# Kernel tuning notes

Measured on AMD Instinct MI355X. Metric: run time of the kernel, lower is better.

Reference implementation:

```python
import jax, jax.numpy as jnp
import numpy as np

B, S, H, NH = 2, 2048, 1024, 16
DK = H // NH

def setup_inputs() -> dict:
    key = jax.random.key(0)
    ks = jax.random.split(key, 12)
    scale = 0.02
    return {
        "Q": jax.random.normal(ks[0], (B, S, H), jnp.float32),
        "K": jax.random.normal(ks[1], (B, S, H), jnp.float32),
        "V": jax.random.normal(ks[2], (B, S, H), jnp.float32),
        "attn_mask": jax.random.randint(ks[3], (B, S, S), 0, 2).astype(bool),
        "Wq": jax.random.normal(ks[4], (H, H), jnp.float32) * scale,
        "bq": jnp.zeros((H,), jnp.float32),
        "Wk": jax.random.normal(ks[5], (H, H), jnp.float32) * scale,
        "bk": jnp.zeros((H,), jnp.float32),
        "Wv": jax.random.normal(ks[6], (H, H), jnp.float32) * scale,
        "bv": jnp.zeros((H,), jnp.float32),
        "Wo": jax.random.normal(ks[7], (H, H), jnp.float32) * scale,
        "bo": jnp.zeros((H,), jnp.float32),
    }

def reference(Q, K, V, attn_mask, Wq, bq, Wk, bk, Wv, bv, Wo, bo):
    b = Q.shape[0]
    # linear projections (torch nn.Linear: x @ W.T + b), split heads -> [b, nh, s, dk]
    def proj(x, W, bias):
        return (x @ W.T + bias).reshape(b, -1, NH, DK).transpose(0, 2, 1, 3)
    q = proj(Q, Wq, bq)
    k = proj(K, Wk, bk)
    v = proj(V, Wv, bv)
    scores = jnp.einsum("bhqd,bhkd->bhqk", q, k) / jnp.sqrt(jnp.float32(DK))
    scores = jnp.where(attn_mask[:, None, :, :], jnp.float32(-1e9), scores)
    attn = jax.nn.softmax(scores, axis=-1)  # dropout prob = 0.0 (identity)
    ctx = jnp.einsum("bhqk,bhkd->bhqd", attn, v)
    ctx = ctx.transpose(0, 2, 1, 3).reshape(b, -1, NH * DK)
    return ctx @ Wo.T + bo
```

## Files before the change

### kernel.cpp

```cpp
#include <hip/hip_runtime.h>

typedef short s16x8 __attribute__((ext_vector_type(8)));
typedef float f32x4 __attribute__((ext_vector_type(4)));
typedef unsigned short u16;
typedef unsigned int u32;
typedef unsigned long long u64;

#define DEVI __device__ __forceinline__

#if __has_builtin(__builtin_amdgcn_exp2f)
#define EXP2F(x) __builtin_amdgcn_exp2f(x)
#else
#define EXP2F(x) exp2f(x)
#endif

#define QSCALE 0.1803368801111204f

DEVI float bf2f(u16 u){ union { u32 i; float f; } v; v.i = ((u32)u) << 16; return v.f; }
DEVI u16 f2bf(float f){ union { float f; u32 i; } v; v.f = f; u32 u = v.i;
                        return (u16)((u + 0x7fffu + ((u >> 16) & 1u)) >> 16); }
DEVI u32 pack2r(float a, float b){
  union { float f; u32 i; } ua, ub; ua.f = a; ub.f = b;
  return ((ua.i + 0x8000u) >> 16) | ((ub.i + 0x8000u) & 0xffff0000u);
}
DEVI u64 pack4(float a, float b, float c, float d){
  return (u64)f2bf(a) | ((u64)f2bf(b) << 16) | ((u64)f2bf(c) << 32) | ((u64)f2bf(d) << 48);
}

DEVI f32x4 mfma_bf16(s16x8 a, s16x8 b, f32x4 c){
  return __builtin_amdgcn_mfma_f32_16x16x32_bf16(a, b, c, 0, 0, 0);
}

#define GLDS(gp, lp) __builtin_amdgcn_global_load_lds( \
    (const __attribute__((address_space(1))) void*)(gp), \
    (__attribute__((address_space(3))) void*)(lp), 16, 0, 0)

DEVI float4 cvt8f32(const float* p){
  float4 x = *(const float4*)p;
  float4 y = *(const float4*)(p + 4);
  union { u16 t[8]; float4 f4; } u;
  u.t[0] = f2bf(x.x); u.t[1] = f2bf(x.y); u.t[2] = f2bf(x.z); u.t[3] = f2bf(x.w);
  u.t[4] = f2bf(y.x); u.t[5] = f2bf(y.y); u.t[6] = f2bf(y.z); u.t[7] = f2bf(y.w);
  return u.f4;
}

DEVI bool detect_f32(const u16* probe){
  __shared__ int dsum[4];
  const int tid = threadIdx.x;
  int bad = 0;
#pragma unroll
  for (int i = 0; i < 16; ++i){
    u16 u = probe[tid * 16 + i];
    int e = (u >> 7) & 0xFF;
    bad += (e != 0 && (e < 100 || e > 150)) ? 1 : 0;
  }
#pragma unroll
  for (int o = 1; o < 64; o <<= 1) bad += __shfl_xor(bad, o);
  if ((tid & 63) == 0) dsum[tid >> 6] = bad;
  __syncthreads();
  bool r = (dsum[0] + dsum[1] + dsum[2] + dsum[3]) > 64;
  __syncthreads();
  return r;
}

struct PrepArgs { const void* src[7]; void* dst[7]; u32 coff[8]; };

__global__ __launch_bounds__(256) void prep_mask(PrepArgs a, const u16* probe,
                                                 const int* __restrict__ mask,
                                                 u64* __restrict__ bits,
                                                 int do_mask, int do_conv){
  if (blockIdx.x < 1024){
    if (!do_mask) return;
    const int lane = threadIdx.x & 63, wid = threadIdx.x >> 6;
    const int row = blockIdx.x * 4 + wid;
    const int* mrow = mask + (size_t)row * 2048;
    for (int c = 0; c < 32; ++c){
      int v = mrow[c * 64 + lane];
      u64 w = __ballot(v == 0);
      if (lane == 0) bits[(size_t)row * 32 + c] = w;
    }
  } else {
    if (!do_conv) return;
    const bool f32 = detect_f32(probe);
    if (!f32) return;
    const u32 total = a.coff[7];
    for (u32 c = (blockIdx.x - 1024) * 256 + threadIdx.x; c < total; c += 2048 * 256){
      int s = 0;
#pragma unroll
      for (int i = 1; i < 7; ++i) s += (c >= a.coff[i]) ? 1 : 0;
      u32 lc = c - a.coff[s];
      ((float4*)a.dst[s])[lc] = cvt8f32((const float*)a.src[s] + (size_t)lc * 8);
    }
  }
}

struct ProjP {
  const void* X[3];   const u16* Xc[3];
  const void* W[3];   const u16* Wc[3];
  const void* bias[3];
  u16* out[3];
  const u16* probe;
  int conv_ok;
};

__global__ __launch_bounds__(256) void proj_gemm(ProjP p){
  __shared__ u16 As[128 * 64];
  __shared__ u16 Bs[128 * 64];
  const int z = blockIdx.z;
  const bool in32 = detect_f32(p.probe);
  const bool f32st = in32 && !p.conv_ok;
  const u16* Ab = (in32 && p.conv_ok) ? p.Xc[z] : (const u16*)p.X[z];
  const u16* Wb = (in32 && p.conv_ok) ? p.Wc[z] : (const u16*)p.W[z];
  const float* Af = (const float*)p.X[z];
  const float* Wf = (const float*)p.W[z];
  const int tid = threadIdx.x;
  const int lane = tid & 63, wid = tid >> 6;
  const int quad = lane >> 4, l15 = lane & 15;
  const int m0 = blockIdx.y * 128, n0 = blockIdx.x * 128;
  const int wm = (wid >> 1) * 64, wn = (wid & 1) * 64;
  const int K = 1024;

  f32x4 acc[4][4];
  const f32x4 z4 = {0.f, 0.f, 0.f, 0.f};
  for (int i = 0; i < 4; ++i) for (int j = 0; j < 4; ++j) acc[i][j] = z4;

  for (int ko = 0; ko < 16; ++ko){
    const int kk = ko * 64;
    if (f32st){
#pragma unroll
      for (int i = 0; i < 4; ++i){
        int g = tid * 4 + i;
        int row = g >> 3, c = g & 7;
        *(float4*)(As + row * 64 + ((c ^ (row & 7)) * 8)) =
            cvt8f32(Af + (size_t)(m0 + row) * K + kk + c * 8);
        *(float4*)(Bs + row * 64 + ((c ^ (row & 7)) * 8)) =
            cvt8f32(Wf + (size_t)(n0 + row) * K + kk + c * 8);
      }
    } else {
#pragma unroll
      for (int i = 0; i < 4; ++i){
        int ci = (wid * 4 + i) * 64 + lane;
        int row = ci >> 3, gcc = (ci & 7) ^ (row & 7);
        GLDS(Ab + (size_t)(m0 + row) * K + kk + gcc * 8, As + (size_t)(wid * 4 + i) * 512);
        GLDS(Wb + (size_t)(n0 + row) * K + kk + gcc * 8, Bs + (size_t)(wid * 4 + i) * 512);
      }
    }
    __syncthreads();
#pragma unroll
    for (int ks = 0; ks < 2; ++ks){
      s16x8 af[4], bfr[4];
#pragma unroll
      for (int mt = 0; mt < 4; ++mt){
        int row = wm + mt * 16 + l15;
        af[mt] = *(const s16x8*)(As + row * 64 + (((ks * 4 + quad) ^ (row & 7)) * 8));
      }
#pragma unroll
      for (int nt = 0; nt < 4; ++nt){
        int row = wn + nt * 16 + l15;
        bfr[nt] = *(const s16x8*)(Bs + row * 64 + (((ks * 4 + quad) ^ (row & 7)) * 8));
      }
#pragma unroll
      for (int mt = 0; mt < 4; ++mt)
#pragma unroll
        for (int nt = 0; nt < 4; ++nt)
          acc[mt][nt] = mfma_bf16(af[mt], bfr[nt], acc[mt][nt]);
    }
    __syncthreads();
  }

  u16* outp = p.out[z];
#pragma unroll
  for (int nt = 0; nt < 4; ++nt){
    int col = n0 + wn + nt * 16 + l15;
    float bv = in32 ? ((const float*)p.bias[z])[col] : bf2f(((const u16*)p.bias[z])[col]);
#pragma unroll
    for (int mt = 0; mt < 4; ++mt){
      if (z == 2){
        int srow = m0 + wm + mt * 16 + quad * 4;
        int b = srow >> 11, s = srow & 2047, hh = col >> 6, d = col & 63;
        size_t idx = (((size_t)(b * 16 + hh)) * 64 + d) * 2048 + s;
        *(u64*)(outp + idx) = pack4(acc[mt][nt][0] + bv, acc[mt][nt][1] + bv,
                                    acc[mt][nt][2] + bv, acc[mt][nt][3] + bv);
      } else {
#pragma unroll
        for (int r = 0; r < 4; ++r){
          int row = m0 + wm + mt * 16 + quad * 4 + r;
          float v = acc[mt][nt][r] + bv;
          if (z == 0) v *= QSCALE;
          int b = row >> 11, s = row & 2047, hh = col >> 6, d = col & 63;
          outp[(((size_t)(b * 16 + hh)) * 2048 + s) * 64 + d] = f2bf(v);
        }
      }
    }
  }
}

__global__ __launch_bounds__(256) void gemm_out(const u16* __restrict__ A,
                                                const void* __restrict__ Wv,
                                                const u16* __restrict__ Wbf,
                                                const void* __restrict__ biasv,
                                                void* __restrict__ outv,
                                                const u16* __restrict__ probe,
                                                int conv_ok){
  __shared__ u16 As[64 * 64];
  __shared__ u16 Bs[64 * 64];
  const bool in32 = detect_f32(probe);
  const bool f32st = in32 && !conv_ok;
  const u16* Wb = (in32 && conv_ok) ? Wbf : (const u16*)Wv;
  const float* Wf = (const float*)Wv;
  const int tid = threadIdx.x;
  const int lane = tid & 63, wid = tid >> 6;
  const int quad = lane >> 4, l15 = lane & 15;
  const int m0 = blockIdx.y * 64, n0 = blockIdx.x * 64;
  const int wm = (wid >> 1) * 32, wn = (wid & 1) * 32;
  const int K = 1024;

  f32x4 acc[2][2];
  const f32x4 z4 = {0.f, 0.f, 0.f, 0.f};
  for (int i = 0; i < 2; ++i) for (int j = 0; j < 2; ++j) acc[i][j] = z4;

  for (int ko = 0; ko < 16; ++ko){
    const int kk = ko * 64;
#pragma unroll
    for (int i = 0; i < 2; ++i){
      int ci = (wid * 2 + i) * 64 + lane;
      int row = ci >> 3, gcc = (ci & 7) ^ (row & 7);
      GLDS(A + (size_t)(m0 + row) * K + kk + gcc * 8, As + (size_t)(wid * 2 + i) * 512);
    }
    if (f32st){
#pragma unroll
      for (int i = 0; i < 2; ++i){
        int g = tid * 2 + i;
        int row = g >> 3, c = g & 7;
        *(float4*)(Bs + row * 64 + ((c ^ (row & 7)) * 8)) =
            cvt8f32(Wf + (size_t)(n0 + row) * K + kk + c * 8);
      }
    } else {
#pragma unroll
      for (int i = 0; i < 2; ++i){
        int ci = (wid * 2 + i) * 64 + lane;
        int row = ci >> 3, gcc = (ci & 7) ^ (row & 7);
        GLDS(Wb + (size_t)(n0 + row) * K + kk + gcc * 8, Bs + (size_t)(wid * 2 + i) * 512);
      }
    }
    __syncthreads();
#pragma unroll
    for (int ks = 0; ks < 2; ++ks){
      s16x8 af[2], bfr[2];
#pragma unroll
      for (int mt = 0; mt < 2; ++mt){
        int row = wm + mt * 16 + l15;
        af[mt] = *(const s16x8*)(As + row * 64 + (((ks * 4 + quad) ^ (row & 7)) * 8));
      }
#pragma unroll
      for (int nt = 0; nt < 2; ++nt){
        int row = wn + nt * 16 + l15;
        bfr[nt] = *(const s16x8*)(Bs + row * 64 + (((ks * 4 + quad) ^ (row & 7)) * 8));
      }
#pragma unroll
      for (int mt = 0; mt < 2; ++mt)
#pragma unroll
        for (int nt = 0; nt < 2; ++nt)
          acc[mt][nt] = mfma_bf16(af[mt], bfr[nt], acc[mt][nt]);
    }
    __syncthreads();
  }

#pragma unroll
  for (int nt = 0; nt < 2; ++nt){
    int col = n0 + wn + nt * 16 + l15;
    float bv = in32 ? ((const float*)biasv)[col] : bf2f(((const u16*)biasv)[col]);
#pragma unroll
    for (int mt = 0; mt < 2; ++mt)
#pragma unroll
      for (int r = 0; r < 4; ++r){
        int row = m0 + wm + mt * 16 + quad * 4 + r;
        float v = acc[mt][nt][r] + bv;
        size_t idx = (size_t)row * 1024 + col;
        if (in32) ((float*)outv)[idx] = v;
        else      ((u16*)outv)[idx]   = f2bf(v);
      }
  }
}

__global__ __launch_bounds__(256) void attn2(const u16* __restrict__ qws,
                                             const u16* __restrict__ kws,
                                             const u16* __restrict__ vtws,
                                             const u64* __restrict__ mbits,
                                             const int* __restrict__ rawmask,
                                             int use_raw,
                                             u16* __restrict__ ctxws){
  __shared__ u16 Ks[64 * 64];
  __shared__ u16 Vt[64 * 64];
  __shared__ u16 Ps[4][16 * 64];
  const int tid = threadIdx.x;
  const int lane = tid & 63, wid = tid >> 6;
  const int quad = lane >> 4, l15 = lane & 15;
  const int h = blockIdx.x, qt = blockIdx.y, b = blockIdx.z;
  const int q0 = qt * 64;
  const size_t bh = (size_t)(b * 16 + h) * (2048 * 64);
  const int qrow = q0 + wid * 16 + l15;

  s16x8 qf[2];
#pragma unroll
  for (int ks = 0; ks < 2; ++ks)
    qf[ks] = *(const s16x8*)(qws + bh + (size_t)qrow * 64 + ks * 32 + quad * 8);

  const f32x4 z4 = {0.f, 0.f, 0.f, 0.f};
  f32x4 ctx[4];
  for (int dt = 0; dt < 4; ++dt) ctx[dt] = z4;
  float lr = 0.f;

  u16* pp = &Ps[wid][0];
  u32 pw[4];
#pragma unroll
  for (int ntk = 0; ntk < 4; ++ntk)
    pw[ntk] = l15 * 64 + (((u32)(ntk * 2 + (quad >> 1)) ^ (u32)(l15 & 7)) * 8) + (quad & 1) * 4;

  const u64* mrow = mbits + ((size_t)(b * 2048 + qrow)) * 32;

  for (int kt = 0; kt < 32; ++kt){
    const int k0 = kt * 64;
#pragma unroll
    for (int i = 0; i < 2; ++i){
      int ci = (wid * 2 + i) * 64 + lane;
      int row = ci >> 3, gcc = (ci & 7) ^ (row & 7);
      GLDS(kws + bh + (size_t)(k0 + row) * 64 + gcc * 8, Ks + (size_t)(wid * 2 + i) * 512);
      GLDS(vtws + bh + (size_t)row * 2048 + k0 + gcc * 8, Vt + (size_t)(wid * 2 + i) * 512);
    }
    __syncthreads();

    f32x4 s[4];
    for (int ntk = 0; ntk < 4; ++ntk) s[ntk] = z4;
#pragma unroll
    for (int ks = 0; ks < 2; ++ks)
#pragma unroll
      for (int ntk = 0; ntk < 4; ++ntk){
        int row = ntk * 16 + l15;
        s16x8 kf = *(const s16x8*)(Ks + row * 64 + (((ks * 4 + quad) ^ (row & 7)) * 8));
        s[ntk] = mfma_bf16(kf, qf[ks], s[ntk]);
      }

    float ls = 0.f;
    if (!use_raw){
      u64 w = mrow[kt] >> (quad * 4);
      u32 wlo = (u32)w, whi = (u32)(w >> 32);
#pragma unroll
      for (int ntk = 0; ntk < 4; ++ntk){
        u32 half = (ntk < 2) ? wlo : whi;
#pragma unroll
        for (int r = 0; r < 4; ++r){
          float pv = EXP2F(s[ntk][r]);
          u32 bit = (half >> ((ntk & 1) * 16 + r)) & 1u;
          pv *= (float)bit;
          s[ntk][r] = pv;
          ls += pv;
        }
      }
    } else {
#pragma unroll
      for (int ntk = 0; ntk < 4; ++ntk)
#pragma unroll
        for (int r = 0; r < 4; ++r){
          int key = k0 + ntk * 16 + quad * 4 + r;
          int mv = rawmask[((size_t)(b * 2048 + qrow)) * 2048 + key];
          float pv = EXP2F(s[ntk][r]);
          pv = mv ? 0.f : pv;
          s[ntk][r] = pv;
          ls += pv;
        }
    }
    lr += ls;

#pragma unroll
    for (int ntk = 0; ntk < 4; ++ntk){
      uint2 t;
      t.x = pack2r(s[ntk][0], s[ntk][1]);
      t.y = pack2r(s[ntk][2], s[ntk][3]);
      *(uint2*)(pp + pw[ntk]) = t;
    }
    s16x8 pf[2];
#pragma unroll
    for (int ks = 0; ks < 2; ++ks)
      pf[ks] = *(const s16x8*)(pp + l15 * 64 + (((ks * 4 + quad) ^ (l15 & 7)) * 8));

#pragma unroll
    for (int ks = 0; ks < 2; ++ks)
#pragma unroll
      for (int dt = 0; dt < 4; ++dt){
        int row = dt * 16 + l15;
        s16x8 vf = *(const s16x8*)(Vt + row * 64 + (((ks * 4 + quad) ^ (row & 7)) * 8));
        ctx[dt] = mfma_bf16(vf, pf[ks], ctx[dt]);
      }
    __syncthreads();
  }

  lr += __shfl_xor(lr, 16);
  lr += __shfl_xor(lr, 32);
  float inv = 1.0f / fmaxf(lr, 1e-30f);

#pragma unroll
  for (int dt = 0; dt < 4; ++dt){
    int d0 = dt * 16 + quad * 4;
    u64 w = pack4(ctx[dt][0] * inv, ctx[dt][1] * inv, ctx[dt][2] * inv, ctx[dt][3] * inv);
    *(u64*)(ctxws + ((size_t)(b * 2048 + qrow)) * 1024 + h * 64 + d0) = w;
  }
}

extern "C" void kernel_launch(void* const* d_in, const int* in_sizes, int n_in,
                              void* d_out, int out_size, void* d_ws, size_t ws_size,
                              hipStream_t stream){
  const void* Q    = d_in[0];
  const void* Kin  = d_in[1];
  const void* Vin  = d_in[2];
  const int* mask  = (const int*)d_in[3];
  const void* Wq = d_in[4];  const void* bq = d_in[5];
  const void* Wk = d_in[6];  const void* bk = d_in[7];
  const void* Wv = d_in[8];  const void* bv = d_in[9];
  const void* Wo = d_in[10]; const void* bo = d_in[11];

  char* ws = (char*)d_ws;
  const size_t MB = 1u << 20;
  const bool small_ws = ws_size < 33 * MB;
  const bool big_ws   = ws_size >= 66 * MB;
  u64* mbits = (u64*)ws;
  const size_t base = small_ws ? 0 : MB;
  u16* qws  = (u16*)(ws + base);
  u16* kws  = (u16*)(ws + base + 8 * MB);
  u16* vtws = (u16*)(ws + base + 16 * MB);
  u16* cws  = (u16*)(ws + base + 24 * MB);
  u16* Qc  = (u16*)(ws + 33 * MB);
  u16* Kc  = (u16*)(ws + 41 * MB);
  u16* Vc  = (u16*)(ws + 49 * MB);
  u16* Wqc = (u16*)(ws + 57 * MB);
  u16* Wkc = (u16*)(ws + 59 * MB);
  u16* Wvc = (u16*)(ws + 61 * MB);
  u16* Woc = (u16*)(ws + 63 * MB);
  const u16* probe = (const u16*)Q;

  PrepArgs pa;
  pa.src[0] = Q;  pa.src[1] = Kin; pa.src[2] = Vin;
  pa.src[3] = Wq; pa.src[4] = Wk;  pa.src[5] = Wv; pa.src[6] = Wo;
  pa.dst[0] = Qc;  pa.dst[1] = Kc;  pa.dst[2] = Vc;
  pa.dst[3] = Wqc; pa.dst[4] = Wkc; pa.dst[5] = Wvc; pa.dst[6] = Woc;
  const u32 cq = 4194304 / 8, cw = 1048576 / 8;
  pa.coff[0] = 0;
  pa.coff[1] = cq;          pa.coff[2] = 2 * cq;      pa.coff[3] = 3 * cq;
  pa.coff[4] = 3 * cq + cw; pa.coff[5] = 3 * cq + 2 * cw;
  pa.coff[6] = 3 * cq + 3 * cw; pa.coff[7] = 3 * cq + 4 * cw;
  prep_mask<<<dim3(3072), 256, 0, stream>>>(pa, probe, mask, mbits,
                                            small_ws ? 0 : 1, big_ws ? 1 : 0);

  ProjP pp;
  pp.X[0] = Q;  pp.X[1] = Kin; pp.X[2] = Vin;
  pp.Xc[0] = Qc; pp.Xc[1] = Kc; pp.Xc[2] = Vc;
  pp.W[0] = Wq; pp.W[1] = Wk; pp.W[2] = Wv;
  pp.Wc[0] = Wqc; pp.Wc[1] = Wkc; pp.Wc[2] = Wvc;
  pp.bias[0] = bq; pp.bias[1] = bk; pp.bias[2] = bv;
  pp.out[0] = qws; pp.out[1] = kws; pp.out[2] = vtws;
  pp.probe = probe;
  pp.conv_ok = big_ws ? 1 : 0;
  proj_gemm<<<dim3(8, 32, 3), 256, 0, stream>>>(pp);

  attn2<<<dim3(16, 32, 2), 256, 0, stream>>>(qws, kws, vtws, mbits, mask,
                                             small_ws ? 1 : 0, cws);

  gemm_out<<<dim3(16, 64), 256, 0, stream>>>(cws, Wo, Woc, bo, d_out, probe,
                                             big_ws ? 1 : 0);
}
```

Baseline: 282.7 us.

## Double-buffer K/V shared tiles in attention to prefetch the next tile

Splits the K and V^T shared-memory tiles into two buffers. The global-to-LDS loads for tile kt+1 are issued right after the barrier at the top of iteration kt, so they overlap with the QK^T, softmax and PV MFMA work on tile kt. The barrier at the end of the loop is removed, leaving one barrier per iteration. This doubles LDS use for K/V, which may reduce occupancy. The compiler may also insert conservative waits on the pending LDS loads that cancel the overlap.

```diff
diff --git a/kernel.cpp b/kernel.cpp
--- a/kernel.cpp
+++ b/kernel.cpp
@@ -290,8 +290,8 @@
                                              const int* __restrict__ rawmask,
                                              int use_raw,
                                              u16* __restrict__ ctxws){
-  __shared__ u16 Ks[64 * 64];
-  __shared__ u16 Vt[64 * 64];
+  __shared__ u16 Ks[2][64 * 64];
+  __shared__ u16 Vt[2][64 * 64];
   __shared__ u16 Ps[4][16 * 64];
   const int tid = threadIdx.x;
   const int lane = tid & 63, wid = tid >> 6;
@@ -319,16 +319,40 @@
 
   const u64* mrow = mbits + ((size_t)(b * 2048 + qrow)) * 32;
 
+  const int sci = wid * 2;
+  int srow0, sgc0, srow1, sgc1;
+  {
+    int ci0 = sci * 64 + lane;
+    srow0 = ci0 >> 3; sgc0 = (ci0 & 7) ^ (srow0 & 7);
+    int ci1 = (sci + 1) * 64 + lane;
+    srow1 = ci1 >> 3; sgc1 = (ci1 & 7) ^ (srow1 & 7);
+  }
+
+  {
+    const int k0 = 0;
+    GLDS(kws + bh + (size_t)(k0 + srow0) * 64 + sgc0 * 8, &Ks[0][0] + (size_t)sci * 512);
+    GLDS(vtws + bh + (size_t)srow0 * 2048 + k0 + sgc0 * 8, &Vt[0][0] + (size_t)sci * 512);
+    GLDS(kws + bh + (size_t)(k0 + srow1) * 64 + sgc1 * 8, &Ks[0][0] + (size_t)(sci + 1) * 512);
+    GLDS(vtws + bh + (size_t)srow1 * 2048 + k0 + sgc1 * 8, &Vt[0][0] + (size_t)(sci + 1) * 512);
+  }
+
   for (int kt = 0; kt < 32; ++kt){
+    const int cur = kt & 1;
+    const u16* kb = &Ks[cur][0];
+    const u16* vb = &Vt[cur][0];
+    __syncthreads();
+
+    if (kt < 31){
+      const int k0n = (kt + 1) * 64;
+      u16* kd = &Ks[cur ^ 1][0];
+      u16* vd = &Vt[cur ^ 1][0];
+      GLDS(kws + bh + (size_t)(k0n + srow0) * 64 + sgc0 * 8, kd + (size_t)sci * 512);
+      GLDS(vtws + bh + (size_t)srow0 * 2048 + k0n + sgc0 * 8, vd + (size_t)sci * 512);
+      GLDS(kws + bh + (size_t)(k0n + srow1) * 64 + sgc1 * 8, kd + (size_t)(sci + 1) * 512);
+      GLDS(vtws + bh + (size_t)srow1 * 2048 + k0n + sgc1 * 8, vd + (size_t)(sci + 1) * 512);
+    }
+
     const int k0 = kt * 64;
-#pragma unroll
-    for (int i = 0; i < 2; ++i){
-      int ci = (wid * 2 + i) * 64 + lane;
-      int row = ci >> 3, gcc = (ci & 7) ^ (row & 7);
-      GLDS(kws + bh + (size_t)(k0 + row) * 64 + gcc * 8, Ks + (size_t)(wid * 2 + i) * 512);
-      GLDS(vtws + bh + (size_t)row * 2048 + k0 + gcc * 8, Vt + (size_t)(wid * 2 + i) * 512);
-    }
-    __syncthreads();
 
     f32x4 s[4];
     for (int ntk = 0; ntk < 4; ++ntk) s[ntk] = z4;
@@ -337,7 +361,7 @@
 #pragma unroll
       for (int ntk = 0; ntk < 4; ++ntk){
         int row = ntk * 16 + l15;
-        s16x8 kf = *(const s16x8*)(Ks + row * 64 + (((ks * 4 + quad) ^ (row & 7)) * 8));
+        s16x8 kf = *(const s16x8*)(kb + row * 64 + (((ks * 4 + quad) ^ (row & 7)) * 8));
         s[ntk] = mfma_bf16(kf, qf[ks], s[ntk]);
       }
 
@@ -389,10 +413,9 @@
 #pragma unroll
       for (int dt = 0; dt < 4; ++dt){
         int row = dt * 16 + l15;
-        s16x8 vf = *(const s16x8*)(Vt + row * 64 + (((ks * 4 + quad) ^ (row & 7)) * 8));
+        s16x8 vf = *(const s16x8*)(vb + row * 64 + (((ks * 4 + quad) ^ (row & 7)) * 8));
         ctx[dt] = mfma_bf16(vf, pf[ks], ctx[dt]);
       }
-    __syncthreads();
   }
 
   lr += __shfl_xor(lr, 16);
```

After: 280.5 us. Within noise of the previous version (-0.8%).
